# Performance work log

Hardware: AMD Instinct MI355X
Metric: run time of the kernel (lower is better)

The kernel has to match this reference:

```python
import jax, jax.numpy as jnp
import numpy as np

B, T, N, D = 16, 1024, 1024, 256   # batch, query len (hp.max_T), key len (hp.max_N), hp.d
WIN = 64                            # hp.attention_win_size
NEG = jnp.float32(-2**32 + 1)       # padding value used by the TF module


def setup_inputs() -> dict:
    key = jax.random.key(0)
    k1, k2, k3, k4 = jax.random.split(key, 4)
    Q = jax.random.normal(k1, (B, T, D), dtype=jnp.float32)
    K = jax.random.normal(k2, (B, N, D), dtype=jnp.float32)
    V = jax.random.normal(k3, (B, N, D), dtype=jnp.float32)
    prev_max_attentions = jax.random.randint(k4, (B,), 0, N - WIN, dtype=jnp.int64)
    return {"Q": Q, "K": K, "V": V, "prev_max_attentions": prev_max_attentions}


def reference(Q, K, V, prev_max_attentions):
    # scaled scores: [B, T, N]
    A = jnp.einsum("btd,bnd->btn", Q, K) * jax.lax.rsqrt(jnp.float32(D))

    # monotonic window mask (mono_attention=True):
    idx = jnp.arange(N)                              # [N]
    prev = prev_max_attentions[:, None]              # [B, 1]
    masks = (idx < prev) | (idx >= prev + WIN)       # [B, N], True = disallowed
    A = jnp.where(masks[:, None, :], NEG, A)         # broadcast over T (== tf.tile)

    A = jax.nn.softmax(A, axis=-1)                   # [B, T, N]
    max_attentions = jnp.argmax(A, axis=-1).astype(jnp.float32)  # [B, T]

    R = jnp.concatenate([jnp.einsum("btn,bnd->btd", A, V), Q], axis=-1)  # [B, T, 2D]
    alignments = jnp.transpose(A, (0, 2, 1))         # [B, N, T]
    return (R, alignments, max_attentions)
```

## Files before the change

### kernel.cpp

```cpp
#include <hip/hip_runtime.h>


#define BB 16
#define TT 1024
#define NN 1024
#define DD 256
#define WIN 64
#define TBLK 16
#define NT 256

#define R_ELEMS   (16u*1024u*512u)
#define ALN_ELEMS (16u*1024u*1024u)

#define LSTR 132

__global__ __launch_bounds__(NT, 4) void attn_v8(
    const float* __restrict__ Q, const float* __restrict__ K,
    const float* __restrict__ V, const int* __restrict__ prev_in,
    float* __restrict__ out)
{
    __shared__ float ks[WIN * LSTR];
    __shared__ float p_lds[TBLK][WIN + 4];

    float* Rout   = out;
    float* aligns = out + R_ELEMS;
    float* maxatt = out + R_ELEMS + ALN_ELEMS;

    const int tid  = threadIdx.x;
    const int lane = tid & 63;
    const int w    = __builtin_amdgcn_readfirstlane(tid >> 6);
    const int b    = blockIdx.x >> 6;
    const int t0   = (blockIdx.x & 63) * TBLK;
    const int prev = prev_in[b];

    const float* qb = Q + ((size_t)b * TT + t0 + 4 * w) * DD;

    float acc[4] = {0.f, 0.f, 0.f, 0.f};
    #pragma unroll
    for (int h = 0; h < 2; ++h) {
        if (h) __syncthreads();
        const float4* Ksrc = (const float4*)(K + ((size_t)b * NN + prev) * DD + h * 128);
        #pragma unroll
        for (int k = 0; k < 8; ++k) {
            int t4 = tid + k * NT;
            int r = t4 >> 5, c = t4 & 31;
            float4 v = Ksrc[(size_t)r * 64 + c];
            *(float4*)&ks[r * LSTR + c * 4] = v;
        }
        __syncthreads();

        const float* qh = qb + h * 128;
        #pragma unroll 8
        for (int d4 = 0; d4 < 32; ++d4) {
            float4 kk = *(const float4*)&ks[lane * LSTR + d4 * 4];
            #pragma unroll
            for (int t = 0; t < 4; ++t) {
                float4 q = ((const float4*)(qh + t * DD))[d4];
                acc[t] = fmaf(q.x, kk.x, fmaf(q.y, kk.y, fmaf(q.z, kk.z, fmaf(q.w, kk.w, acc[t]))));
            }
        }
    }

    #pragma unroll
    for (int t = 0; t < 4; ++t) {
        float v = acc[t] * 0.0625f;

        float m = v;
        #pragma unroll
        for (int off = 32; off; off >>= 1) m = fmaxf(m, __shfl_xor(m, off));

        float e = expf(v - m);
        float s = e;
        #pragma unroll
        for (int off = 32; off; off >>= 1) s += __shfl_xor(s, off);

        p_lds[4 * w + t][lane] = e / s;

        float av = v; int ai = lane;
        #pragma unroll
        for (int off = 32; off; off >>= 1) {
            float ov = __shfl_xor(av, off);
            int   oi = __shfl_xor(ai, off);
            if (ov > av || (ov == av && oi < ai)) { av = ov; ai = oi; }
        }
        if (lane == 0) maxatt[(size_t)b * TT + t0 + 4 * w + t] = (float)(prev + ai);
    }
    __syncthreads();

    {
        const int j = tid >> 2, cg = tid & 3;
        float4 v;
        v.x = p_lds[cg * 4 + 0][j];
        v.y = p_lds[cg * 4 + 1][j];
        v.z = p_lds[cg * 4 + 2][j];
        v.w = p_lds[cg * 4 + 3][j];
        *(float4*)(aligns + ((size_t)b * NN + prev + j) * TT + t0 + cg * 4) = v;
    }

    {
        const int chunk = blockIdx.x & 63;
        float4* zbase = (float4*)(aligns + (size_t)b * NN * TT);
        const float4 z = make_float4(0.f, 0.f, 0.f, 0.f);
        #pragma unroll
        for (int r = 0; r < 15; ++r) {
            int idx = chunk * 15 + r;
            int n   = idx < prev ? idx : idx + WIN;
            zbase[(size_t)n * 256 + tid] = z;
        }
    }

    {
        const float4* V4 = (const float4*)(V + ((size_t)b * NN + prev) * DD);
        float4 o[4];
        #pragma unroll
        for (int t = 0; t < 4; ++t) o[t] = make_float4(0.f, 0.f, 0.f, 0.f);

        #pragma unroll 4
        for (int j4 = 0; j4 < WIN / 4; ++j4) {
            float4 p0 = *(const float4*)&p_lds[4 * w + 0][j4 * 4];
            float4 p1 = *(const float4*)&p_lds[4 * w + 1][j4 * 4];
            float4 p2 = *(const float4*)&p_lds[4 * w + 2][j4 * 4];
            float4 p3 = *(const float4*)&p_lds[4 * w + 3][j4 * 4];
            float4 v0 = V4[(size_t)(j4 * 4 + 0) * 64 + lane];
            float4 v1 = V4[(size_t)(j4 * 4 + 1) * 64 + lane];
            float4 v2 = V4[(size_t)(j4 * 4 + 2) * 64 + lane];
            float4 v3 = V4[(size_t)(j4 * 4 + 3) * 64 + lane];
            #define ACC4(o_, p_) \
                o_.x = fmaf(p_.x, v0.x, fmaf(p_.y, v1.x, fmaf(p_.z, v2.x, fmaf(p_.w, v3.x, o_.x)))); \
                o_.y = fmaf(p_.x, v0.y, fmaf(p_.y, v1.y, fmaf(p_.z, v2.y, fmaf(p_.w, v3.y, o_.y)))); \
                o_.z = fmaf(p_.x, v0.z, fmaf(p_.y, v1.z, fmaf(p_.z, v2.z, fmaf(p_.w, v3.z, o_.z)))); \
                o_.w = fmaf(p_.x, v0.w, fmaf(p_.y, v1.w, fmaf(p_.z, v2.w, fmaf(p_.w, v3.w, o_.w))));
            ACC4(o[0], p0) ACC4(o[1], p1) ACC4(o[2], p2) ACC4(o[3], p3)
            #undef ACC4
        }

        #pragma unroll
        for (int t = 0; t < 4; ++t) {
            float* Rrow = Rout + ((size_t)b * TT + t0 + 4 * w + t) * (2 * DD);
            ((float4*)Rrow)[lane] = o[t];
            ((float4*)(Rrow + DD))[lane] = ((const float4*)(qb + t * DD))[lane];
        }
    }
}

extern "C" void kernel_launch(void* const* d_in, const int* in_sizes, int n_in,
                              void* d_out, int out_size, void* d_ws, size_t ws_size,
                              hipStream_t stream) {
    const float* Q = (const float*)d_in[0];
    const float* K = (const float*)d_in[1];
    const float* V = (const float*)d_in[2];
    const int* prev = (const int*)d_in[3];
    float* out = (float*)d_out;

    attn_v8<<<BB * TT / TBLK, NT, 0, stream>>>(Q, K, V, prev, out);
}
```

Baseline: 165.9 us.

## Split QK dot product across waves by head dimension with register-held K

The QK score stage is restructured. Each wave now covers a 64-wide slice of the head dimension for all 16 query rows of the block, instead of 4 rows over the full dimension. Each lane keeps its K row slice in registers, so the K tile is no longer staged through LDS and the two staging barriers go away. Partial sums are reduced through a small LDS buffer with a single barrier. The alignment strip is written straight from registers, which drops the transpose pass through p_lds and its barrier. The trade-offs are more registers for 16 accumulators plus K, and per-lane strided K reads in place of coalesced tile loads.

```diff
diff --git a/kernel.cpp b/kernel.cpp
--- a/kernel.cpp
+++ b/kernel.cpp
@@ -12,14 +12,12 @@
 #define R_ELEMS   (16u*1024u*512u)
 #define ALN_ELEMS (16u*1024u*1024u)
 
-#define LSTR 132
-
-__global__ __launch_bounds__(NT, 4) void attn_v8(
+__global__ __launch_bounds__(NT, 4) void attn_v9(
     const float* __restrict__ Q, const float* __restrict__ K,
     const float* __restrict__ V, const int* __restrict__ prev_in,
     float* __restrict__ out)
 {
-    __shared__ float ks[WIN * LSTR];
+    __shared__ float part[4][TBLK][64];
     __shared__ float p_lds[TBLK][WIN + 4];
 
     float* Rout   = out;
@@ -33,37 +31,40 @@
     const int t0   = (blockIdx.x & 63) * TBLK;
     const int prev = prev_in[b];
 
-    const float* qb = Q + ((size_t)b * TT + t0 + 4 * w) * DD;
+    {
+        const float4* Kq = (const float4*)(K + ((size_t)b * NN + prev + lane) * DD + w * 64);
+        const float*  Qw = Q + ((size_t)b * TT + t0) * DD + w * 64;
 
-    float acc[4] = {0.f, 0.f, 0.f, 0.f};
-    #pragma unroll
-    for (int h = 0; h < 2; ++h) {
-        if (h) __syncthreads();
-        const float4* Ksrc = (const float4*)(K + ((size_t)b * NN + prev) * DD + h * 128);
+        float acc[TBLK];
         #pragma unroll
-        for (int k = 0; k < 8; ++k) {
-            int t4 = tid + k * NT;
-            int r = t4 >> 5, c = t4 & 31;
-            float4 v = Ksrc[(size_t)r * 64 + c];
-            *(float4*)&ks[r * LSTR + c * 4] = v;
-        }
-        __syncthreads();
+        for (int t = 0; t < TBLK; ++t) acc[t] = 0.f;
 
-        const float* qh = qb + h * 128;
-        #pragma unroll 8
-        for (int d4 = 0; d4 < 32; ++d4) {
-            float4 kk = *(const float4*)&ks[lane * LSTR + d4 * 4];
+        #pragma unroll
+        for (int c = 0; c < 2; ++c) {
+            float4 kreg[8];
             #pragma unroll
-            for (int t = 0; t < 4; ++t) {
-                float4 q = ((const float4*)(qh + t * DD))[d4];
-                acc[t] = fmaf(q.x, kk.x, fmaf(q.y, kk.y, fmaf(q.z, kk.z, fmaf(q.w, kk.w, acc[t]))));
+            for (int d4 = 0; d4 < 8; ++d4) kreg[d4] = Kq[c * 8 + d4];
+            #pragma unroll
+            for (int t = 0; t < TBLK; ++t) {
+                #pragma unroll
+                for (int d4 = 0; d4 < 8; ++d4) {
+                    float4 q = ((const float4*)(Qw + t * DD))[c * 8 + d4];
+                    acc[t] = fmaf(q.x, kreg[d4].x, fmaf(q.y, kreg[d4].y,
+                             fmaf(q.z, kreg[d4].z, fmaf(q.w, kreg[d4].w, acc[t]))));
+                }
             }
         }
+        #pragma unroll
+        for (int t = 0; t < TBLK; ++t) part[w][t][lane] = acc[t];
     }
+    __syncthreads();
 
+    float4 strip;
     #pragma unroll
-    for (int t = 0; t < 4; ++t) {
-        float v = acc[t] * 0.0625f;
+    for (int tt = 0; tt < 4; ++tt) {
+        const int t = 4 * w + tt;
+        float v = (part[0][t][lane] + part[1][t][lane] +
+                   part[2][t][lane] + part[3][t][lane]) * 0.0625f;
 
         float m = v;
         #pragma unroll
@@ -74,7 +75,9 @@
         #pragma unroll
         for (int off = 32; off; off >>= 1) s += __shfl_xor(s, off);
 
-        p_lds[4 * w + t][lane] = e / s;
+        float pv = e / s;
+        p_lds[t][lane] = pv;
+        ((float*)&strip)[tt] = pv;
 
         float av = v; int ai = lane;
         #pragma unroll
@@ -83,19 +86,10 @@
             int   oi = __shfl_xor(ai, off);
             if (ov > av || (ov == av && oi < ai)) { av = ov; ai = oi; }
         }
-        if (lane == 0) maxatt[(size_t)b * TT + t0 + 4 * w + t] = (float)(prev + ai);
+        if (lane == 0) maxatt[(size_t)b * TT + t0 + t] = (float)(prev + ai);
     }
-    __syncthreads();
 
-    {
-        const int j = tid >> 2, cg = tid & 3;
-        float4 v;
-        v.x = p_lds[cg * 4 + 0][j];
-        v.y = p_lds[cg * 4 + 1][j];
-        v.z = p_lds[cg * 4 + 2][j];
-        v.w = p_lds[cg * 4 + 3][j];
-        *(float4*)(aligns + ((size_t)b * NN + prev + j) * TT + t0 + cg * 4) = v;
-    }
+    *(float4*)(aligns + ((size_t)b * NN + prev + lane) * TT + t0 + 4 * w) = strip;
 
     {
         const int chunk = blockIdx.x & 63;
@@ -110,6 +104,7 @@
     }
 
     {
+        const float* qb = Q + ((size_t)b * TT + t0 + 4 * w) * DD;
         const float4* V4 = (const float4*)(V + ((size_t)b * NN + prev) * DD);
         float4 o[4];
         #pragma unroll
@@ -152,5 +147,5 @@
     const int* prev = (const int*)d_in[3];
     float* out = (float*)d_out;
 
-    attn_v8<<<BB * TT / TBLK, NT, 0, stream>>>(Q, K, V, prev, out);
+    attn_v9<<<BB * TT / TBLK, NT, 0, stream>>>(Q, K, V, prev, out);
 }
```

Measured after the change: 174.9 us. 5.4% more time.
